# Optimization experiments

Hardware: AMD Instinct MI355X
Metric: run time of the kernel (lower is better)

## Reference

```python
import jax, jax.numpy as jnp
from jax import lax
import numpy as np

C = 256
K = 3
PAD = 1


def _bilinear_sample(x, py, px):
    """Zero-padded bilinear sampling.
    x: [B,C,Hin,Win]; py,px: [B,Kt,H,W] float sample coords -> [B,C,Kt,H,W]."""
    B, Cc, Hin, Win = x.shape
    y0 = jnp.floor(py)
    x0 = jnp.floor(px)
    y1 = y0 + 1.0
    x1 = x0 + 1.0
    wy1 = py - y0
    wy0 = 1.0 - wy1
    wx1 = px - x0
    wx0 = 1.0 - wx1
    xf = x.reshape(B, Cc, Hin * Win)

    def corner(yi, xi, wy, wx):
        valid = (yi >= 0) & (yi < Hin) & (xi >= 0) & (xi < Win)
        yc = jnp.clip(yi, 0, Hin - 1).astype(jnp.int32)
        xc = jnp.clip(xi, 0, Win - 1).astype(jnp.int32)
        idx = yc * Win + xc  # [B,Kt,H,W]
        g = jax.vmap(lambda xb, ib: xb[:, ib])(xf, idx)  # [B,C,Kt,H,W]
        w = (wy * wx) * valid.astype(x.dtype)
        return g * w[:, None]

    return (corner(y0, x0, wy0, wx0) + corner(y0, x1, wy0, wx1)
            + corner(y1, x0, wy1, wx0) + corner(y1, x1, wy1, wx1))


def _arm_forward(x, w_off, b_off, w, b):
    B, Cc, H, W = x.shape
    # offset-predicting conv (standard 3x3, pad 1)
    off = lax.conv_general_dilated(
        x, w_off, window_strides=(1, 1), padding=[(PAD, PAD), (PAD, PAD)],
        dimension_numbers=('NCHW', 'OIHW', 'NCHW')) + b_off[None, :, None, None]
    off = off.reshape(B, K * K, 2, H, W)  # [:, k, 0]=dy, [:, k, 1]=dx (mmcv layout)
    ky, kx = jnp.meshgrid(jnp.arange(K), jnp.arange(K), indexing='ij')
    ky = ky.reshape(-1).astype(x.dtype)  # [9]
    kx = kx.reshape(-1).astype(x.dtype)
    base_y = jnp.arange(H, dtype=x.dtype)[None, None, :, None]
    base_x = jnp.arange(W, dtype=x.dtype)[None, None, None, :]
    py = base_y - PAD + ky[None, :, None, None] + off[:, :, 0]  # [B,9,H,W]
    px = base_x - PAD + kx[None, :, None, None] + off[:, :, 1]
    sampled = _bilinear_sample(x, py, px)  # [B,C,9,H,W]
    out = jnp.einsum('bckhw,ock->bohw', sampled, w.reshape(Cc, Cc, K * K))
    out = out + b[None, :, None, None]
    return jax.nn.sigmoid(out)


def setup_inputs() -> dict:
    key = jax.random.key(0)
    k1, k2, k3, k4 = jax.random.split(key, 4)
    B, H, W = 8, 64, 64
    x = jax.random.normal(k1, (B, C, H, W), dtype=jnp.float32)
    # offset conv params (mmcv zero-inits these; use small random to exercise sampling)
    w_off = jax.random.normal(k2, (2 * K * K, C, K, K), dtype=jnp.float32) * 0.01
    b_off = jnp.zeros((2 * K * K,), dtype=jnp.float32)
    # deformable conv weight/bias (kaiming-ish scale)
    scale = 1.0 / np.sqrt(C * K * K)
    w = jax.random.normal(k3, (C, C, K, K), dtype=jnp.float32) * scale
    b = jax.random.normal(k4, (C,), dtype=jnp.float32) * scale
    return {"Fstagei": x, "w_off": w_off, "b_off": b_off, "w": w, "b": b}


def reference(Fstagei, w_off, b_off, w, b):
    return _arm_forward(Fstagei, w_off, b_off, w, b)
```

## Files before the change

kernel.cpp:

```cpp
#include <hip/hip_runtime.h>

typedef unsigned short u16;
typedef unsigned int u32;
typedef __attribute__((ext_vector_type(8))) short short8;
typedef __attribute__((ext_vector_type(4))) float f32x4;

#define BB 8
#define CCH 256
#define HH 64
#define WW 64
#define HP 66
#define NPOS 4096
#define KTOT 2304

#define XT_BYTES   17842176ull
#define W2R_OFF    17842176ull
#define WOFF2_OFF  19021824ull
#define P_OFF      19169280ull
#define OFF2_OFF   40402944ull
#define WS_MIN     42762240ull

__device__ __forceinline__ float bf2f(u16 u) {
    union { u32 u; float f; } v; v.u = ((u32)u) << 16; return v.f;
}
__device__ __forceinline__ u16 f2bf(float f) {
    union { float f; u32 u; } v; v.f = f;
    u32 r = v.u + 0x7FFFu + ((v.u >> 16) & 1u);
    return (u16)(r >> 16);
}
__device__ __forceinline__ u32 pk2(float a, float b) {
    return (u32)f2bf(a) | ((u32)f2bf(b) << 16);
}
__device__ __forceinline__ void bf2x2(u32 p, float& a, float& b) {
    union { u32 u; float f; } va, vb;
    va.u = p << 16; vb.u = p & 0xffff0000u;
    a = va.f; b = vb.f;
}
__device__ __forceinline__ void ldg_lds16(const u16* g, u16* l) {
    __builtin_amdgcn_global_load_lds((const __attribute__((address_space(1))) u32*)g,
                                     (__attribute__((address_space(3))) u32*)l, 16, 0, 0);
}

__global__ __launch_bounds__(256) void k_pre(const float* __restrict__ w, const float* __restrict__ w_off,
                                             const float* __restrict__ x,
                                             u16* __restrict__ W2r, u16* __restrict__ Woff2,
                                             u16* __restrict__ xT) {
    __shared__ __align__(16) float SH[4608];
    int bx = blockIdx.x;
    int t = threadIdx.x;
    if (bx < 256) {
        int o = bx;
        const float* src = w + (size_t)o * 2304;
#pragma unroll
        for (int j = 0; j < 9; ++j) SH[j * 256 + t] = src[j * 256 + t];
        __syncthreads();
        u16* dst = W2r + (size_t)o * 2304;
#pragma unroll
        for (int k = 0; k < 9; ++k) dst[k * 256 + t] = f2bf(SH[t * 9 + k]);
    } else if (bx == 256) {
        for (int o2 = 0; o2 < 32; ++o2) {
            if (o2 < 18) {
                const float* src = w_off + (size_t)o2 * 2304;
#pragma unroll
                for (int j = 0; j < 9; ++j) SH[j * 256 + t] = src[j * 256 + t];
                __syncthreads();
#pragma unroll
                for (int k = 0; k < 9; ++k) Woff2[(size_t)o2 * 2304 + k * 256 + t] = f2bf(SH[t * 9 + k]);
                __syncthreads();
            } else {
#pragma unroll
                for (int k = 0; k < 9; ++k) Woff2[(size_t)o2 * 2304 + k * 256 + t] = 0;
            }
        }
    } else if (bx < 777) {
        int idx = (bx - 257) * 4 + (t >> 6);
        int b = idx / 260, m = idx - b * 260;
        int y, xx;
        if (m < 66)       { y = 0;  xx = m; }
        else if (m < 132) { y = 65; xx = m - 66; }
        else if (m < 196) { y = m - 132 + 1; xx = 0; }
        else              { y = m - 196 + 1; xx = 65; }
        u16* p = xT + ((size_t)(b * HP + y) * HP + xx) * CCH + (t & 63) * 4;
        uint2 zz; zz.x = 0; zz.y = 0;
        *(uint2*)p = zz;
    } else {
        int idx = bx - 777;
        int b = idx & 7;
        int r = idx >> 3;
        int y = r & 63, c0 = (r >> 6) * 64;
        {
            int i = t >> 2, seg = t & 3;
            const float* src = x + (((size_t)(b * CCH + c0 + i) * HH + y) * WW) + seg * 16;
            float4 v0 = *(const float4*)(src);
            float4 v1 = *(const float4*)(src + 4);
            float4 v2 = *(const float4*)(src + 8);
            float4 v3 = *(const float4*)(src + 12);
            *(float4*)&SH[i * 72 + seg * 16]      = v0;
            *(float4*)&SH[i * 72 + seg * 16 + 4]  = v1;
            *(float4*)&SH[i * 72 + seg * 16 + 8]  = v2;
            *(float4*)&SH[i * 72 + seg * 16 + 12] = v3;
        }
        __syncthreads();
        {
            int xc = t >> 2, cs = t & 3;
            u16* dst = xT + (((size_t)(b * HP + y + 1) * HP) + (xc + 1)) * CCH + c0 + cs * 16;
            u32 p[8];
#pragma unroll
            for (int j = 0; j < 8; ++j)
                p[j] = pk2(SH[(cs * 16 + 2 * j) * 72 + xc], SH[(cs * 16 + 2 * j + 1) * 72 + xc]);
            uint4 d0, d1;
            d0.x = p[0]; d0.y = p[1]; d0.z = p[2]; d0.w = p[3];
            d1.x = p[4]; d1.y = p[5]; d1.z = p[6]; d1.w = p[7];
            *(uint4*)dst = d0;
            *(uint4*)(dst + 8) = d1;
        }
    }
}

__global__ __launch_bounds__(256) void k_offconv(const u16* __restrict__ xT,
                                                 const u16* __restrict__ Woff2,
                                                 float* __restrict__ P) {
    __shared__ __align__(16) u16 AS[2][2048];
    __shared__ __align__(16) u16 BS[2][8192];
    int b = blockIdx.x, k9 = blockIdx.y;
    int pos0 = blockIdx.z * 128;
    int ky = k9 / 3, kx = k9 % 3;
    int t = threadIdx.x, lane = t & 63, wv = t >> 6;

    int srow = lane >> 3;
    int sw8 = ((lane & 7) ^ srow) << 3;
    const u16* pA = Woff2 + (size_t)k9 * 256;
    const u16* pXb = xT + (size_t)b * HP * HP * CCH;

    f32x4 acc[2][2];
    f32x4 z = {0.f, 0.f, 0.f, 0.f};
    acc[0][0] = z; acc[0][1] = z; acc[1][0] = z; acc[1][1] = z;

    auto stage = [&](int cs, int d) {
        int koff = cs * 64;
        {
            int row = wv * 8 + srow;
            ldg_lds16(pA + (size_t)row * KTOT + koff + sw8, &AS[d][wv * 512]);
        }
#pragma unroll
        for (int i = 0; i < 4; ++i) {
            int inst = wv * 4 + i;
            int rowg = pos0 + inst * 8 + srow;
            int py_ = rowg >> 6, px_ = rowg & 63;
            const u16* g = pXb + (((size_t)(py_ + ky) * HP) + px_ + kx) * CCH + koff + sw8;
            ldg_lds16(g, &BS[d][inst * 512]);
        }
    };

    stage(0, 0);
    __syncthreads();

    int buf = 0;
    int m = lane & 15, q = lane >> 4, key = lane & 7;
    for (int cs = 0; cs < 4; ++cs) {
        if (cs < 3) stage(cs + 1, buf ^ 1);
#pragma unroll
        for (int j = 0; j < 2; ++j) {
            int slot8 = (((j * 4 + q) ^ key) << 3);
            short8 a0 = *(const short8*)&AS[buf][m * 64 + slot8];
            short8 a1 = *(const short8*)&AS[buf][(16 + m) * 64 + slot8];
            short8 b0 = *(const short8*)&BS[buf][(wv * 32 + m) * 64 + slot8];
            short8 b1 = *(const short8*)&BS[buf][(wv * 32 + 16 + m) * 64 + slot8];
            acc[0][0] = __builtin_amdgcn_mfma_f32_16x16x32_bf16(a0, b0, acc[0][0], 0, 0, 0);
            acc[0][1] = __builtin_amdgcn_mfma_f32_16x16x32_bf16(a0, b1, acc[0][1], 0, 0, 0);
            acc[1][0] = __builtin_amdgcn_mfma_f32_16x16x32_bf16(a1, b0, acc[1][0], 0, 0, 0);
            acc[1][1] = __builtin_amdgcn_mfma_f32_16x16x32_bf16(a1, b1, acc[1][1], 0, 0, 0);
        }
        __syncthreads();
        buf ^= 1;
    }
    int nn = lane & 15;
    float* Pp = P + (size_t)(b * 9 + k9) * 18 * NPOS;
#pragma unroll
    for (int ao = 0; ao < 2; ++ao)
#pragma unroll
        for (int bn = 0; bn < 2; ++bn) {
            int pos = pos0 + wv * 32 + bn * 16 + nn;
#pragma unroll
            for (int r = 0; r < 4; ++r) {
                int o = ao * 16 + q * 4 + r;
                if (o < 18) Pp[o * NPOS + pos] = acc[ao][bn][r];
            }
        }
}

__global__ __launch_bounds__(256) void k_reduce(const float* __restrict__ P,
                                                const float* __restrict__ b_off,
                                                float2* __restrict__ off2) {
    int b = blockIdx.x;
    int pos = blockIdx.y * 256 + threadIdx.x;
    float s[18];
#pragma unroll
    for (int o = 0; o < 18; ++o) s[o] = b_off[o];
    const float* Pp = P + (size_t)(b * 9) * 18 * NPOS + pos;
    for (int k9 = 0; k9 < 9; ++k9) {
#pragma unroll
        for (int o = 0; o < 18; ++o)
            s[o] += Pp[(k9 * 18 + o) * NPOS];
    }
#pragma unroll
    for (int op = 0; op < 9; ++op) {
        float2 v; v.x = s[2 * op]; v.y = s[2 * op + 1];
        off2[(((size_t)(b * 9 + op)) << 12) + pos] = v;
    }
}

__global__ __launch_bounds__(512, 2) void k_gemm(const u16* __restrict__ xT,
                                                 const float2* __restrict__ off2,
                                                 const u16* __restrict__ W2r,
                                                 const float* __restrict__ bias,
                                                 float* __restrict__ out) {
    __shared__ __align__(16) u16 AS[2][16384];
    __shared__ __align__(16) u16 BSF[128 * 264];
    int b = blockIdx.x;
    int pos0 = blockIdx.z * 128;
    int t = threadIdx.x, lane = t & 63, wv = t >> 6;
    int wr = wv >> 1, wc = wv & 1;

    int srow = lane >> 3;
    int sw8 = ((lane & 7) ^ srow) << 3;
    const u16* pA = W2r;

    int g = t >> 4, ll = t & 15;
    int bbase = b * HP * HP;

    f32x4 acc[4][4];
    f32x4 z = {0.f, 0.f, 0.f, 0.f};
#pragma unroll
    for (int i = 0; i < 4; ++i)
#pragma unroll
        for (int j = 0; j < 4; ++j) acc[i][j] = z;

    auto stageA = [&](int gs, int d) {
        int k9 = gs >> 2, cs = gs & 3;
        int koffA = k9 * 256 + cs * 64;
#pragma unroll
        for (int i = 0; i < 4; ++i) {
            int inst = wv * 4 + i;
            int row = inst * 8 + srow;
            ldg_lds16(pA + (size_t)row * KTOT + koffA + sw8, &AS[d][inst * 512]);
        }
    };

    stageA(0, 0);

    int m = lane & 15, q = lane >> 4, key = lane & 7;
    for (int t9 = 0; t9 < 9; ++t9) {
        int ky = t9 / 3, kx = t9 - (t9 / 3) * 3;
#pragma unroll
        for (int i = 0; i < 4; ++i) {
            int pos = pos0 + g + i * 32;
            int y = pos >> 6, x = pos & 63;
            float2 off = off2[(((size_t)(b * 9 + t9)) << 12) + pos];
            float pyf = (float)(y - 1 + ky) + off.x;
            float pxf = (float)(x - 1 + kx) + off.y;
            float y0f = floorf(pyf), x0f = floorf(pxf);
            int y0 = (int)y0f, x0 = (int)x0f;
            int y1 = y0 + 1, x1 = x0 + 1;
            float wy1 = pyf - y0f, wy0 = 1.f - wy1;
            float wx1 = pxf - x0f, wx0 = 1.f - wx1;
            bool vy0 = (y0 >= 0) & (y0 < HH), vy1 = (y1 >= 0) & (y1 < HH);
            bool vx0 = (x0 >= 0) & (x0 < WW), vx1 = (x1 >= 0) & (x1 < WW);
            int yc0 = min(max(y0, 0), HH - 1), yc1 = min(max(y1, 0), HH - 1);
            int xc0 = min(max(x0, 0), WW - 1), xc1 = min(max(x1, 0), WW - 1);
            float w0 = (vy0 & vx0) ? wy0 * wx0 : 0.f;
            float w1 = (vy0 & vx1) ? wy0 * wx1 : 0.f;
            float w2 = (vy1 & vx0) ? wy1 * wx0 : 0.f;
            float w3 = (vy1 & vx1) ? wy1 * wx1 : 0.f;
            const u16* g0 = xT + (size_t)((bbase + (yc0 + 1) * HP + xc0 + 1)) * CCH;
            const u16* g1 = xT + (size_t)((bbase + (yc0 + 1) * HP + xc1 + 1)) * CCH;
            const u16* g2 = xT + (size_t)((bbase + (yc1 + 1) * HP + xc0 + 1)) * CCH;
            const u16* g3 = xT + (size_t)((bbase + (yc1 + 1) * HP + xc1 + 1)) * CCH;
            int row = g + i * 32;
            u16* sp = &BSF[row * 264];
#pragma unroll
            for (int cp = 0; cp < 2; ++cp) {
                int c = cp * 128 + ll * 8;
                uint4 r0 = *(const uint4*)(g0 + c);
                uint4 r1 = *(const uint4*)(g1 + c);
                uint4 r2 = *(const uint4*)(g2 + c);
                uint4 r3 = *(const uint4*)(g3 + c);
                float v[8];
#pragma unroll
                for (int dw = 0; dw < 4; ++dw) {
                    u32 p0 = ((const u32*)&r0)[dw];
                    u32 p1 = ((const u32*)&r1)[dw];
                    u32 p2 = ((const u32*)&r2)[dw];
                    u32 p3 = ((const u32*)&r3)[dw];
                    float a0, b0_, a1, b1_, a2, b2_, a3, b3_;
                    bf2x2(p0, a0, b0_);
                    bf2x2(p1, a1, b1_);
                    bf2x2(p2, a2, b2_);
                    bf2x2(p3, a3, b3_);
                    v[2 * dw]     = w0 * a0 + w1 * a1 + w2 * a2 + w3 * a3;
                    v[2 * dw + 1] = w0 * b0_ + w1 * b1_ + w2 * b2_ + w3 * b3_;
                }
                uint4 sv;
                sv.x = pk2(v[0], v[1]); sv.y = pk2(v[2], v[3]);
                sv.z = pk2(v[4], v[5]); sv.w = pk2(v[6], v[7]);
                *(uint4*)(sp + c) = sv;
            }
        }
        asm volatile("s_waitcnt lgkmcnt(0)" ::: "memory");
        __builtin_amdgcn_s_barrier();
#pragma unroll
        for (int cs = 0; cs < 4; ++cs) {
            int gs = t9 * 4 + cs;
            int cur = gs & 1;
            if (gs < 35) {
                stageA(gs + 1, cur ^ 1);
                asm volatile("s_waitcnt vmcnt(4)" ::: "memory");
            } else {
                asm volatile("s_waitcnt vmcnt(0)" ::: "memory");
            }
            __builtin_amdgcn_s_barrier();
#pragma unroll
            for (int j = 0; j < 2; ++j) {
                int slot8 = (((j * 4 + q) ^ key) << 3);
                int bchunk = (cs * 8 + j * 4 + q) << 3;
                short8 af[4], bfr[4];
#pragma unroll
                for (int ao = 0; ao < 4; ++ao)
                    af[ao] = *(const short8*)&AS[cur][(wr * 64 + ao * 16 + m) * 64 + slot8];
#pragma unroll
                for (int bn = 0; bn < 4; ++bn)
                    bfr[bn] = *(const short8*)&BSF[(wc * 64 + bn * 16 + m) * 264 + bchunk];
                __builtin_amdgcn_s_setprio(1);
#pragma unroll
                for (int ao = 0; ao < 4; ++ao)
#pragma unroll
                    for (int bn = 0; bn < 4; ++bn)
                        acc[ao][bn] = __builtin_amdgcn_mfma_f32_16x16x32_bf16(af[ao], bfr[bn], acc[ao][bn], 0, 0, 0);
                __builtin_amdgcn_s_setprio(0);
            }
            __builtin_amdgcn_s_barrier();
        }
    }

    int nn = lane & 15;
#pragma unroll
    for (int ao = 0; ao < 4; ++ao) {
        int ob = wr * 64 + ao * 16 + q * 4;
#pragma unroll
        for (int bn = 0; bn < 4; ++bn) {
            int pos = pos0 + wc * 64 + bn * 16 + nn;
#pragma unroll
            for (int r = 0; r < 4; ++r) {
                float v = acc[ao][bn][r] + bias[ob + r];
                float sg = 1.0f / (1.0f + __expf(-v));
                out[(size_t)((b * CCH + ob + r) * NPOS) + pos] = sg;
            }
        }
    }
}

extern "C" void kernel_launch(void* const* d_in, const int* in_sizes, int n_in,
                              void* d_out, int out_size, void* d_ws, size_t ws_size,
                              hipStream_t stream) {
    const float* x     = (const float*)d_in[0];
    const float* w_off = (const float*)d_in[1];
    const float* b_off = (const float*)d_in[2];
    const float* w     = (const float*)d_in[3];
    const float* bias  = (const float*)d_in[4];
    float* out = (float*)d_out;

    char* ws = (char*)d_ws;
    u16*    xT    = (u16*)ws;
    u16*    W2r   = (u16*)(ws + W2R_OFF);
    u16*    Woff2 = (u16*)(ws + WOFF2_OFF);
    float*  P     = (float*)(ws + P_OFF);
    float2* off2  = (float2*)(ws + OFF2_OFF);

    if (ws_size < WS_MIN) return;

    k_pre<<<2825, 256, 0, stream>>>(w, w_off, x, W2r, Woff2, xT);
    k_offconv<<<dim3(8, 9, 32), 256, 0, stream>>>(xT, Woff2, P);
    k_reduce<<<dim3(8, 16), 256, 0, stream>>>(P, b_off, off2);
    k_gemm<<<dim3(8, 1, 32), 512, 0, stream>>>(xT, off2, W2r, bias, out);
}
```

Before: 200.1 us.

## Software-pipeline deformable bilinear gather with MFMA across channel sub-steps

The bilinear gather for the next kernel tap is split into four channel regions. Its global loads are issued one sub-step ahead and blended into the single B tile while MFMAs run on the current region. Offset loads and sample-state computation are also hoisted one tap ahead, and there is now one barrier per sub-step instead of two. The blend packing switches from software rounding to the hardware v_cvt_pk_bf16_f32 instruction. The cost is more live registers for the in-flight gather data and hand-tuned vmcnt waits, which could hurt occupancy or correctness if the counts are off.

```diff
diff --git a/kernel.cpp b/kernel.cpp
--- a/kernel.cpp
+++ b/kernel.cpp
@@ -30,6 +30,11 @@
 }
 __device__ __forceinline__ u32 pk2(float a, float b) {
     return (u32)f2bf(a) | ((u32)f2bf(b) << 16);
+}
+__device__ __forceinline__ u32 cvtpk(float lo, float hi) {
+    u32 r;
+    asm("v_cvt_pk_bf16_f32 %0, %1, %2" : "=v"(r) : "v"(lo), "v"(hi));
+    return r;
 }
 __device__ __forceinline__ void bf2x2(u32 p, float& a, float& b) {
     union { u32 u; float f; } va, vb;
@@ -226,7 +231,8 @@
     int sw8 = ((lane & 7) ^ srow) << 3;
     const u16* pA = W2r;
 
-    int g = t >> 4, ll = t & 15;
+    int brow0 = t >> 3;
+    int bcl = (t & 7) << 3;
     int bbase = b * HP * HP;
 
     f32x4 acc[4][4];
@@ -247,18 +253,19 @@
         }
     };
 
-    stageA(0, 0);
-
-    int m = lane & 15, q = lane >> 4, key = lane & 7;
-    for (int t9 = 0; t9 < 9; ++t9) {
-        int ky = t9 / 3, kx = t9 - (t9 / 3) * 3;
-#pragma unroll
-        for (int i = 0; i < 4; ++i) {
-            int pos = pos0 + g + i * 32;
+    const u16* gp[2][4];
+    float wt[2][4];
+    float2 fnext[2];
+    uint4 gv[8];
+
+    auto computeState = [&](int tap) {
+#pragma unroll
+        for (int ii = 0; ii < 2; ++ii) {
+            int pos = pos0 + brow0 + (ii << 6);
             int y = pos >> 6, x = pos & 63;
-            float2 off = off2[(((size_t)(b * 9 + t9)) << 12) + pos];
-            float pyf = (float)(y - 1 + ky) + off.x;
-            float pxf = (float)(x - 1 + kx) + off.y;
+            int ky = tap / 3, kx = tap - (tap / 3) * 3;
+            float pyf = (float)(y - 1 + ky) + fnext[ii].x;
+            float pxf = (float)(x - 1 + kx) + fnext[ii].y;
             float y0f = floorf(pyf), x0f = floorf(pxf);
             int y0 = (int)y0f, x0 = (int)x0f;
             int y1 = y0 + 1, x1 = x0 + 1;
@@ -268,78 +275,104 @@
             bool vx0 = (x0 >= 0) & (x0 < WW), vx1 = (x1 >= 0) & (x1 < WW);
             int yc0 = min(max(y0, 0), HH - 1), yc1 = min(max(y1, 0), HH - 1);
             int xc0 = min(max(x0, 0), WW - 1), xc1 = min(max(x1, 0), WW - 1);
-            float w0 = (vy0 & vx0) ? wy0 * wx0 : 0.f;
-            float w1 = (vy0 & vx1) ? wy0 * wx1 : 0.f;
-            float w2 = (vy1 & vx0) ? wy1 * wx0 : 0.f;
-            float w3 = (vy1 & vx1) ? wy1 * wx1 : 0.f;
-            const u16* g0 = xT + (size_t)((bbase + (yc0 + 1) * HP + xc0 + 1)) * CCH;
-            const u16* g1 = xT + (size_t)((bbase + (yc0 + 1) * HP + xc1 + 1)) * CCH;
-            const u16* g2 = xT + (size_t)((bbase + (yc1 + 1) * HP + xc0 + 1)) * CCH;
-            const u16* g3 = xT + (size_t)((bbase + (yc1 + 1) * HP + xc1 + 1)) * CCH;
-            int row = g + i * 32;
-            u16* sp = &BSF[row * 264];
-#pragma unroll
-            for (int cp = 0; cp < 2; ++cp) {
-                int c = cp * 128 + ll * 8;
-                uint4 r0 = *(const uint4*)(g0 + c);
-                uint4 r1 = *(const uint4*)(g1 + c);
-                uint4 r2 = *(const uint4*)(g2 + c);
-                uint4 r3 = *(const uint4*)(g3 + c);
-                float v[8];
-#pragma unroll
-                for (int dw = 0; dw < 4; ++dw) {
-                    u32 p0 = ((const u32*)&r0)[dw];
-                    u32 p1 = ((const u32*)&r1)[dw];
-                    u32 p2 = ((const u32*)&r2)[dw];
-                    u32 p3 = ((const u32*)&r3)[dw];
-                    float a0, b0_, a1, b1_, a2, b2_, a3, b3_;
-                    bf2x2(p0, a0, b0_);
-                    bf2x2(p1, a1, b1_);
-                    bf2x2(p2, a2, b2_);
-                    bf2x2(p3, a3, b3_);
-                    v[2 * dw]     = w0 * a0 + w1 * a1 + w2 * a2 + w3 * a3;
-                    v[2 * dw + 1] = w0 * b0_ + w1 * b1_ + w2 * b2_ + w3 * b3_;
-                }
-                uint4 sv;
-                sv.x = pk2(v[0], v[1]); sv.y = pk2(v[2], v[3]);
-                sv.z = pk2(v[4], v[5]); sv.w = pk2(v[6], v[7]);
-                *(uint4*)(sp + c) = sv;
+            wt[ii][0] = (vy0 & vx0) ? wy0 * wx0 : 0.f;
+            wt[ii][1] = (vy0 & vx1) ? wy0 * wx1 : 0.f;
+            wt[ii][2] = (vy1 & vx0) ? wy1 * wx0 : 0.f;
+            wt[ii][3] = (vy1 & vx1) ? wy1 * wx1 : 0.f;
+            gp[ii][0] = xT + (size_t)(bbase + (yc0 + 1) * HP + xc0 + 1) * CCH + bcl;
+            gp[ii][1] = xT + (size_t)(bbase + (yc0 + 1) * HP + xc1 + 1) * CCH + bcl;
+            gp[ii][2] = xT + (size_t)(bbase + (yc1 + 1) * HP + xc0 + 1) * CCH + bcl;
+            gp[ii][3] = xT + (size_t)(bbase + (yc1 + 1) * HP + xc1 + 1) * CCH + bcl;
+        }
+    };
+    auto gatherRegion = [&](int rr) {
+#pragma unroll
+        for (int ii = 0; ii < 2; ++ii)
+#pragma unroll
+            for (int c = 0; c < 4; ++c)
+                gv[ii * 4 + c] = *(const uint4*)(gp[ii][c] + rr * 64);
+    };
+    auto blendWrite = [&](int rr) {
+#pragma unroll
+        for (int ii = 0; ii < 2; ++ii) {
+            int row = brow0 + (ii << 6);
+            float v[8];
+#pragma unroll
+            for (int dw = 0; dw < 4; ++dw) {
+                float a0, b0_, a1, b1_, a2, b2_, a3, b3_;
+                bf2x2(((const u32*)&gv[ii * 4 + 0])[dw], a0, b0_);
+                bf2x2(((const u32*)&gv[ii * 4 + 1])[dw], a1, b1_);
+                bf2x2(((const u32*)&gv[ii * 4 + 2])[dw], a2, b2_);
+                bf2x2(((const u32*)&gv[ii * 4 + 3])[dw], a3, b3_);
+                v[2 * dw]     = wt[ii][0] * a0 + wt[ii][1] * a1 + wt[ii][2] * a2 + wt[ii][3] * a3;
+                v[2 * dw + 1] = wt[ii][0] * b0_ + wt[ii][1] * b1_ + wt[ii][2] * b2_ + wt[ii][3] * b3_;
             }
-        }
+            uint4 sv;
+            sv.x = cvtpk(v[0], v[1]); sv.y = cvtpk(v[2], v[3]);
+            sv.z = cvtpk(v[4], v[5]); sv.w = cvtpk(v[6], v[7]);
+            *(uint4*)&BSF[row * 264 + rr * 64 + bcl] = sv;
+        }
+    };
+
+    {
+        fnext[0] = off2[((size_t)(b * 9 + 0) << 12) + pos0 + brow0];
+        fnext[1] = off2[((size_t)(b * 9 + 0) << 12) + pos0 + brow0 + 64];
+        computeState(0);
+#pragma unroll
+        for (int rr = 0; rr < 4; ++rr) {
+            gatherRegion(rr);
+            blendWrite(rr);
+        }
+        fnext[0] = off2[((size_t)(b * 9 + 1) << 12) + pos0 + brow0];
+        fnext[1] = off2[((size_t)(b * 9 + 1) << 12) + pos0 + brow0 + 64];
+        stageA(0, 0);
         asm volatile("s_waitcnt lgkmcnt(0)" ::: "memory");
+    }
+
+    int m = lane & 15, q = lane >> 4, key = lane & 7;
+    for (int gs = 0; gs <= 35; ++gs) {
+        int t9 = gs >> 2, cs = gs & 3, cur = gs & 1;
+        if (gs >= 1 && gs <= 32) { asm volatile("s_waitcnt vmcnt(8)" ::: "memory"); }
+        else                     { asm volatile("s_waitcnt vmcnt(0)" ::: "memory"); }
         __builtin_amdgcn_s_barrier();
-#pragma unroll
-        for (int cs = 0; cs < 4; ++cs) {
-            int gs = t9 * 4 + cs;
-            int cur = gs & 1;
-            if (gs < 35) {
-                stageA(gs + 1, cur ^ 1);
-                asm volatile("s_waitcnt vmcnt(4)" ::: "memory");
-            } else {
-                asm volatile("s_waitcnt vmcnt(0)" ::: "memory");
+
+        if (gs < 35) stageA(gs + 1, cur ^ 1);
+        __builtin_amdgcn_sched_barrier(0);
+
+        if (gs >= 1 && gs <= 32) {
+            asm volatile("s_waitcnt vmcnt(4)" ::: "memory");
+            blendWrite((cs + 3) & 3);
+        }
+        if (cs == 0 && t9 <= 7) computeState(t9 + 1);
+        if (gs <= 31) {
+            if (cs == 3 && t9 <= 6) {
+                fnext[0] = off2[((size_t)(b * 9 + t9 + 2) << 12) + pos0 + brow0];
+                fnext[1] = off2[((size_t)(b * 9 + t9 + 2) << 12) + pos0 + brow0 + 64];
             }
-            __builtin_amdgcn_s_barrier();
-#pragma unroll
-            for (int j = 0; j < 2; ++j) {
-                int slot8 = (((j * 4 + q) ^ key) << 3);
-                int bchunk = (cs * 8 + j * 4 + q) << 3;
-                short8 af[4], bfr[4];
-#pragma unroll
-                for (int ao = 0; ao < 4; ++ao)
-                    af[ao] = *(const short8*)&AS[cur][(wr * 64 + ao * 16 + m) * 64 + slot8];
+            gatherRegion(cs);
+        }
+        __builtin_amdgcn_sched_barrier(0);
+
+#pragma unroll
+        for (int j = 0; j < 2; ++j) {
+            int slot8 = (((j * 4 + q) ^ key) << 3);
+            int bchunk = (cs * 8 + j * 4 + q) << 3;
+            short8 af[4], bfr[4];
+#pragma unroll
+            for (int ao = 0; ao < 4; ++ao)
+                af[ao] = *(const short8*)&AS[cur][(wr * 64 + ao * 16 + m) * 64 + slot8];
+#pragma unroll
+            for (int bn = 0; bn < 4; ++bn)
+                bfr[bn] = *(const short8*)&BSF[(wc * 64 + bn * 16 + m) * 264 + bchunk];
+            __builtin_amdgcn_s_setprio(1);
+#pragma unroll
+            for (int ao = 0; ao < 4; ++ao)
 #pragma unroll
                 for (int bn = 0; bn < 4; ++bn)
-                    bfr[bn] = *(const short8*)&BSF[(wc * 64 + bn * 16 + m) * 264 + bchunk];
-                __builtin_amdgcn_s_setprio(1);
-#pragma unroll
-                for (int ao = 0; ao < 4; ++ao)
-#pragma unroll
-                    for (int bn = 0; bn < 4; ++bn)
-                        acc[ao][bn] = __builtin_amdgcn_mfma_f32_16x16x32_bf16(af[ao], bfr[bn], acc[ao][bn], 0, 0, 0);
-                __builtin_amdgcn_s_setprio(0);
-            }
-            __builtin_amdgcn_s_barrier();
-        }
+                    acc[ao][bn] = __builtin_amdgcn_mfma_f32_16x16x32_bf16(af[ao], bfr[bn], acc[ao][bn], 0, 0, 0);
+            __builtin_amdgcn_s_setprio(0);
+        }
+        asm volatile("s_waitcnt lgkmcnt(0)" ::: "memory");
     }
 
     int nn = lane & 15;
```

Result: faster. 185.7 us (-7.2%).
